# Kernel optimization log

Hardware: AMD Instinct MI355X
Metric: run time of the kernel (lower is better)

## Reference

```python
import jax, jax.numpy as jnp
import numpy as np

B, H, W, C = 4, 256, 256, 256
WS = 8          # window size (both dims)
HEADS = 1
SEQ = WS * WS   # 64 tokens per window
NW = B * (H // WS) * (W // WS)  # 4096 windows
INNER = C * HEADS


def setup_inputs() -> dict:
    key = jax.random.key(0)
    k1, k2, k3, k4 = jax.random.split(key, 4)
    x = jax.random.normal(k1, (B, H, W, C), dtype=jnp.float32)
    attn = jax.random.uniform(k2, (NW, HEADS, SEQ, SEQ), dtype=jnp.float32)
    # to_v: Linear(dim, inner_dim, bias=False); stored as [in, out] for x @ Wv
    Wv = jax.random.normal(k3, (C, INNER), dtype=jnp.float32) * (C ** -0.5)
    # to_out: Linear(inner_dim, dim)
    Wo = jax.random.normal(k4, (INNER, C), dtype=jnp.float32) * (INNER ** -0.5)
    bo = jnp.zeros((C,), dtype=jnp.float32)
    return {"x": x, "attn": attn, "Wv": Wv, "Wo": Wo, "bo": bo}


def reference(x, attn, Wv, Wo, bo):
    b, h, w, c = x.shape
    nh, nw = h // WS, w // WS
    # window partition: b (h b0) (w b1) c -> (b h w) (b0 b1) c
    xw = x.reshape(b, nh, WS, nw, WS, c).transpose(0, 1, 3, 2, 4, 5)
    xw = xw.reshape(b * nh * nw, SEQ, c)
    # value projection, split heads: n s (h d) -> n h s d
    v = (xw @ Wv).reshape(-1, SEQ, HEADS, c).transpose(0, 2, 1, 3)
    # precomputed-attention weighted sum
    out = jnp.einsum('nhij,nhjd->nhid', attn, v)
    # merge heads: n h s d -> n s (h d)
    out = out.transpose(0, 2, 1, 3).reshape(-1, SEQ, HEADS * c)
    out = out @ Wo + bo
    # window un-partition: (b h w) (b0 b1) c -> b (h b0) (w b1) c
    out = out.reshape(b, nh, nw, WS, WS, c).transpose(0, 1, 3, 2, 4, 5)
    return out.reshape(b, h, w, c)
```

## Files before the change

kernel.cpp:

```cpp
#include <hip/hip_runtime.h>
#include <hip/hip_bf16.h>


typedef __bf16 bf16x8 __attribute__((ext_vector_type(8)));
typedef __bf16 bf16x4 __attribute__((ext_vector_type(4)));
typedef float  f32x16 __attribute__((ext_vector_type(16)));
typedef float  f32x4  __attribute__((ext_vector_type(4)));
typedef unsigned int uint;
typedef uint   uint4v __attribute__((ext_vector_type(4)));

#define MFMA32(a, b, c) __builtin_amdgcn_mfma_f32_32x32x16_bf16(a, b, c, 0, 0, 0)

__global__ void wfuse_kernel(const float* __restrict__ Wv,
                             const float* __restrict__ Wo,
                             __bf16* __restrict__ WT) {
  const int n = blockIdx.x;
  const int k = threadIdx.x;
  const float* wvrow = Wv + k * 256;
  float acc = 0.f;
#pragma unroll 4
  for (int j = 0; j < 256; j += 4) {
    f32x4 wv = *(const f32x4*)(wvrow + j);
    acc += wv.x * Wo[(j + 0) * 256 + n];
    acc += wv.y * Wo[(j + 1) * 256 + n];
    acc += wv.z * Wo[(j + 2) * 256 + n];
    acc += wv.w * Wo[(j + 3) * 256 + n];
  }
  WT[n * 256 + k] = (__bf16)acc;
}

static __device__ __forceinline__ uint pkbf(float lo, float hi) {
  return (uint)__builtin_bit_cast(unsigned short, (__bf16)lo) |
         ((uint)__builtin_bit_cast(unsigned short, (__bf16)hi) << 16);
}

static __device__ __forceinline__ void build_bfrags(const f32x16 acc, int lh,
                                                    bf16x8* bf) {
  uint wd0 = pkbf(acc[0],  acc[1]);
  uint wd1 = pkbf(acc[2],  acc[3]);
  uint wd2 = pkbf(acc[4],  acc[5]);
  uint wd3 = pkbf(acc[6],  acc[7]);
  uint wd4 = pkbf(acc[8],  acc[9]);
  uint wd5 = pkbf(acc[10], acc[11]);
  uint wd6 = pkbf(acc[12], acc[13]);
  uint wd7 = pkbf(acc[14], acc[15]);
  {
    uint o0 = (uint)__shfl_xor((int)wd2, 32);
    uint o1 = (uint)__shfl_xor((int)wd3, 32);
    uint o2 = (uint)__shfl_xor((int)wd0, 32);
    uint o3 = (uint)__shfl_xor((int)wd1, 32);
    uint4v uv = { lh ? o0 : wd0, lh ? o1 : wd1,
                  lh ? wd2 : o2, lh ? wd3 : o3 };
    bf[0] = __builtin_bit_cast(bf16x8, uv);
  }
  {
    uint o0 = (uint)__shfl_xor((int)wd6, 32);
    uint o1 = (uint)__shfl_xor((int)wd7, 32);
    uint o2 = (uint)__shfl_xor((int)wd4, 32);
    uint o3 = (uint)__shfl_xor((int)wd5, 32);
    uint4v uv = { lh ? o0 : wd4, lh ? o1 : wd5,
                  lh ? wd6 : o2, lh ? wd7 : o3 };
    bf[1] = __builtin_bit_cast(bf16x8, uv);
  }
}

static __device__ __forceinline__ long wbase(int w) {
  int wi = w & 31;
  int hi = (w >> 5) & 31;
  int b  = w >> 10;
  return (((long)(b * 256 + hi * 8)) * 256 + wi * 8) * 256;
}

static __device__ __forceinline__ void dma16(const float* gp, char* lp) {
  __builtin_amdgcn_global_load_lds(
      (const __attribute__((address_space(1))) uint*)gp,
      (__attribute__((address_space(3))) uint*)lp, 16, 0, 0);
}

static __device__ __forceinline__ bf16x8 ldax_h(const char* xs, int tok, int g) {
  const int sw = tok & 31;
  f32x4 u = *(const f32x4*)(xs + tok * 512 + ((g ^ sw) << 4));
  f32x4 v = *(const f32x4*)(xs + tok * 512 + (((g + 1) ^ sw) << 4));
  bf16x8 r;
  r[0] = (__bf16)u.x; r[1] = (__bf16)u.y; r[2] = (__bf16)u.z; r[3] = (__bf16)u.w;
  r[4] = (__bf16)v.x; r[5] = (__bf16)v.y; r[6] = (__bf16)v.z; r[7] = (__bf16)v.w;
  return r;
}

__global__ __launch_bounds__(512, 2)
void na_msa_kernel(const float* __restrict__ x,
                   const float* __restrict__ attn,
                   const __bf16* __restrict__ WT,
                   const float* __restrict__ bo,
                   float* __restrict__ out) {
  __shared__ char lds[81920];

  const int t    = threadIdx.x;
  const int lane = t & 63;
  const int wvi  = t >> 6;
  const int ln31 = lane & 31;
  const int lh   = lane >> 5;

  const __bf16* wtp = WT + (wvi * 32 + ln31) * 256 + 8 * lh;
  const float bv = bo[wvi * 32 + ln31];

  const int arow0 = t >> 4;
  const int ak0   = (t & 15) * 4;

  const int w0 = blockIdx.x * 8;

#define STAGE_XH(W, HALF, BUFOFF) do {                                     \
    const float* xp_ = x + wbase(W);                                       \
    _Pragma("unroll")                                                      \
    for (int jj = 0; jj < 4; ++jj) {                                       \
      int tp_ = jj * 8 + wvi;                                              \
      int tok_ = tp_ * 2 + (lane >> 5);                                    \
      int perm_ = (lane & 31) ^ (tok_ & 31);                               \
      const float* gp_ = xp_ + (tok_ >> 3) * 65536 + (tok_ & 7) * 256 +    \
                         (HALF) * 128 + perm_ * 4;                         \
      int off_ = __builtin_amdgcn_readfirstlane((BUFOFF) + tp_ * 1024);    \
      dma16(gp_, lds + off_);                                              \
    } } while (0)

#define AWR(BAT, R0, R1) do {                                              \
    *(bf16x4*)((BAT) + arow0 * 128 + ((ak0 * 2) ^ ((arow0 & 7) << 4))) =   \
        bf16x4{ (__bf16)(R0).x, (__bf16)(R0).y, (__bf16)(R0).z, (__bf16)(R0).w }; \
    int row1_ = 32 + arow0;                                                \
    *(bf16x4*)((BAT) + row1_ * 128 + ((ak0 * 2) ^ ((row1_ & 7) << 4))) =   \
        bf16x4{ (__bf16)(R1).x, (__bf16)(R1).y, (__bf16)(R1).z, (__bf16)(R1).w }; \
    } while (0)

  bf16x8 wb[16];
#pragma unroll
  for (int ks = 0; ks < 16; ++ks) wb[ks] = *(const bf16x8*)(wtp + ks * 16);

  {
    const float* ap = attn + (long)w0 * 4096;
    f32x4 a0 = *(const f32x4*)(ap + t * 4);
    f32x4 a1 = *(const f32x4*)(ap + (512 + t) * 4);
    STAGE_XH(w0, 0, 0);
    AWR(lds + 65536, a0, a1);
  }
  asm volatile("s_waitcnt vmcnt(0) lgkmcnt(0)" ::: "memory");
  __builtin_amdgcn_s_barrier();
  __builtin_amdgcn_sched_barrier(0);

#pragma unroll 1
  for (int i = 0; i < 8; ++i) {
    const int w = w0 + i;
    const char* as = lds + 65536 + (i & 1) * 8192;

    f32x4 ra0, ra1;
    if (i < 7) {
      const float* ap = attn + (long)(w + 1) * 4096;
      ra0 = *(const f32x4*)(ap + t * 4);
      ra1 = *(const f32x4*)(ap + (512 + t) * 4);
    }
    STAGE_XH(w, 1, 32768);
    __builtin_amdgcn_sched_barrier(0);

    f32x16 acc0 = {}, acc1 = {};
#pragma unroll
    for (int ks = 0; ks < 8; ++ks) {
      int g = 4 * ks + 2 * lh;
      bf16x8 a0 = ldax_h(lds, ln31, g);
      bf16x8 a1 = ldax_h(lds, 32 + ln31, g);
      acc0 = MFMA32(a0, wb[ks], acc0);
      acc1 = MFMA32(a1, wb[ks], acc1);
    }
    asm volatile("s_waitcnt vmcnt(0) lgkmcnt(0)" ::: "memory");
    __builtin_amdgcn_s_barrier();
    __builtin_amdgcn_sched_barrier(0);

    if (i < 7) STAGE_XH(w + 1, 0, 0);
    __builtin_amdgcn_sched_barrier(0);

#pragma unroll
    for (int ks = 8; ks < 16; ++ks) {
      int g = 4 * (ks - 8) + 2 * lh;
      bf16x8 a0 = ldax_h(lds + 32768, ln31, g);
      bf16x8 a1 = ldax_h(lds + 32768, 32 + ln31, g);
      acc0 = MFMA32(a0, wb[ks], acc0);
      acc1 = MFMA32(a1, wb[ks], acc1);
    }

    bf16x8 bfr[4];
    build_bfrags(acc0, lh, &bfr[0]);
    build_bfrags(acc1, lh, &bfr[2]);

    if (i < 7) {
      AWR(lds + 65536 + ((i + 1) & 1) * 8192, ra0, ra1);
    }

    float* op = out + wbase(w);
    const int ch = wvi * 32 + ln31;

    {
      f32x16 o0 = {};
#pragma unroll
      for (int ks = 0; ks < 4; ++ks) {
        int kk = ks * 16 + 8 * lh;
        int ab0 = ln31 * 128 + ((kk * 2) ^ ((ln31 & 7) << 4));
        bf16x8 a0 = *(const bf16x8*)(as + ab0);
        o0 = MFMA32(a0, bfr[ks], o0);
      }
#pragma unroll
      for (int r = 0; r < 16; ++r) {
        int tok = (r & 3) + 8 * (r >> 2) + 4 * lh;
        op[(tok >> 3) * 65536 + (tok & 7) * 256 + ch] = o0[r] + bv;
      }
    }
    {
      f32x16 o1 = {};
#pragma unroll
      for (int ks = 0; ks < 4; ++ks) {
        int kk = ks * 16 + 8 * lh;
        int ab0 = ln31 * 128 + ((kk * 2) ^ ((ln31 & 7) << 4));
        bf16x8 a1 = *(const bf16x8*)(as + ab0 + 4096);
        o1 = MFMA32(a1, bfr[ks], o1);
      }
#pragma unroll
      for (int r = 0; r < 16; ++r) {
        int tok = 32 + (r & 3) + 8 * (r >> 2) + 4 * lh;
        op[(tok >> 3) * 65536 + (tok & 7) * 256 + ch] = o1[r] + bv;
      }
    }

    asm volatile("s_waitcnt vmcnt(32) lgkmcnt(0)" ::: "memory");
    __builtin_amdgcn_s_barrier();
    __builtin_amdgcn_sched_barrier(0);
  }
#undef STAGE_XH
#undef AWR
}

extern "C" void kernel_launch(void* const* d_in, const int* in_sizes, int n_in,
                              void* d_out, int out_size, void* d_ws, size_t ws_size,
                              hipStream_t stream) {
  const float* x    = (const float*)d_in[0];
  const float* attn = (const float*)d_in[1];
  const float* Wv   = (const float*)d_in[2];
  const float* Wo   = (const float*)d_in[3];
  const float* bo   = (const float*)d_in[4];
  float* out = (float*)d_out;
  __bf16* WT = (__bf16*)d_ws;

  wfuse_kernel<<<256, 256, 0, stream>>>(Wv, Wo, WT);
  na_msa_kernel<<<512, 512, 0, stream>>>(x, attn, WT, bo, out);
}
```

Measured before the change: 151.3 us.

## Triple-buffer x halves and DMA attn into LDS, 16 windows per block

Replaces the register-staged attention load with direct global-to-LDS DMA kept in fp32 and converted to bf16 at read time. The x half-tiles now rotate through three LDS buffers, so the next window's prefetch overlaps more of the current compute, with tuned vmcnt waits. Each block processes 16 windows over half as many blocks, and LDS grows to 128KB. This likely allows only one block per CU, lowering occupancy, and adds fp32-to-bf16 conversion work on the attention operand reads.

```diff
diff --git a/kernel.cpp b/kernel.cpp
--- a/kernel.cpp
+++ b/kernel.cpp
@@ -3,7 +3,6 @@
 
 
 typedef __bf16 bf16x8 __attribute__((ext_vector_type(8)));
-typedef __bf16 bf16x4 __attribute__((ext_vector_type(4)));
 typedef float  f32x16 __attribute__((ext_vector_type(16)));
 typedef float  f32x4  __attribute__((ext_vector_type(4)));
 typedef unsigned int uint;
@@ -32,6 +31,13 @@
 static __device__ __forceinline__ uint pkbf(float lo, float hi) {
   return (uint)__builtin_bit_cast(unsigned short, (__bf16)lo) |
          ((uint)__builtin_bit_cast(unsigned short, (__bf16)hi) << 16);
+}
+
+static __device__ __forceinline__ bf16x8 cvt8(f32x4 u, f32x4 v) {
+  bf16x8 r;
+  r[0] = (__bf16)u.x; r[1] = (__bf16)u.y; r[2] = (__bf16)u.z; r[3] = (__bf16)u.w;
+  r[4] = (__bf16)v.x; r[5] = (__bf16)v.y; r[6] = (__bf16)v.z; r[7] = (__bf16)v.w;
+  return r;
 }
 
 static __device__ __forceinline__ void build_bfrags(const f32x16 acc, int lh,
@@ -81,10 +87,14 @@
   const int sw = tok & 31;
   f32x4 u = *(const f32x4*)(xs + tok * 512 + ((g ^ sw) << 4));
   f32x4 v = *(const f32x4*)(xs + tok * 512 + (((g + 1) ^ sw) << 4));
-  bf16x8 r;
-  r[0] = (__bf16)u.x; r[1] = (__bf16)u.y; r[2] = (__bf16)u.z; r[3] = (__bf16)u.w;
-  r[4] = (__bf16)v.x; r[5] = (__bf16)v.y; r[6] = (__bf16)v.z; r[7] = (__bf16)v.w;
-  return r;
+  return cvt8(u, v);
+}
+
+static __device__ __forceinline__ bf16x8 ldat(const char* as, int row, int g) {
+  const int sw = row & 15;
+  f32x4 u = *(const f32x4*)(as + row * 256 + ((g ^ sw) << 4));
+  f32x4 v = *(const f32x4*)(as + row * 256 + (((g + 1) ^ sw) << 4));
+  return cvt8(u, v);
 }
 
 __global__ __launch_bounds__(512, 2)
@@ -93,7 +103,7 @@
                    const __bf16* __restrict__ WT,
                    const float* __restrict__ bo,
                    float* __restrict__ out) {
-  __shared__ char lds[81920];
+  __shared__ char lds[131072];
 
   const int t    = threadIdx.x;
   const int lane = t & 63;
@@ -104,10 +114,7 @@
   const __bf16* wtp = WT + (wvi * 32 + ln31) * 256 + 8 * lh;
   const float bv = bo[wvi * 32 + ln31];
 
-  const int arow0 = t >> 4;
-  const int ak0   = (t & 15) * 4;
-
-  const int w0 = blockIdx.x * 8;
+  const int w0 = blockIdx.x * 16;
 
 #define STAGE_XH(W, HALF, BUFOFF) do {                                     \
     const float* xp_ = x + wbase(W);                                       \
@@ -122,64 +129,69 @@
       dma16(gp_, lds + off_);                                              \
     } } while (0)
 
-#define AWR(BAT, R0, R1) do {                                              \
-    *(bf16x4*)((BAT) + arow0 * 128 + ((ak0 * 2) ^ ((arow0 & 7) << 4))) =   \
-        bf16x4{ (__bf16)(R0).x, (__bf16)(R0).y, (__bf16)(R0).z, (__bf16)(R0).w }; \
-    int row1_ = 32 + arow0;                                                \
-    *(bf16x4*)((BAT) + row1_ * 128 + ((ak0 * 2) ^ ((row1_ & 7) << 4))) =   \
-        bf16x4{ (__bf16)(R1).x, (__bf16)(R1).y, (__bf16)(R1).z, (__bf16)(R1).w }; \
-    } while (0)
+#define STAGE_AT(W, BUFOFF) do {                                           \
+    const float* ap_ = attn + (long)(W) * 4096;                            \
+    _Pragma("unroll")                                                      \
+    for (int jj = 0; jj < 2; ++jj) {                                       \
+      int j_ = wvi * 2 + jj;                                               \
+      int row_ = j_ * 4 + (lane >> 4);                                     \
+      int g_ = (lane & 15) ^ (row_ & 15);                                  \
+      const float* gp_ = ap_ + row_ * 64 + g_ * 4;                         \
+      int off_ = __builtin_amdgcn_readfirstlane((BUFOFF) + j_ * 1024);     \
+      dma16(gp_, lds + off_);                                              \
+    } } while (0)
 
   bf16x8 wb[16];
 #pragma unroll
   for (int ks = 0; ks < 16; ++ks) wb[ks] = *(const bf16x8*)(wtp + ks * 16);
 
-  {
-    const float* ap = attn + (long)w0 * 4096;
-    f32x4 a0 = *(const f32x4*)(ap + t * 4);
-    f32x4 a1 = *(const f32x4*)(ap + (512 + t) * 4);
-    STAGE_XH(w0, 0, 0);
-    AWR(lds + 65536, a0, a1);
-  }
+  STAGE_XH(w0, 0, 0);
+  STAGE_AT(w0, 98304);
+  STAGE_XH(w0, 1, 32768);
   asm volatile("s_waitcnt vmcnt(0) lgkmcnt(0)" ::: "memory");
   __builtin_amdgcn_s_barrier();
   __builtin_amdgcn_sched_barrier(0);
 
+  int rA = 0, rB = 32768, rC = 65536;
+
 #pragma unroll 1
-  for (int i = 0; i < 8; ++i) {
+  for (int i = 0; i < 16; ++i) {
     const int w = w0 + i;
-    const char* as = lds + 65536 + (i & 1) * 8192;
-
-    f32x4 ra0, ra1;
-    if (i < 7) {
-      const float* ap = attn + (long)(w + 1) * 4096;
-      ra0 = *(const f32x4*)(ap + t * 4);
-      ra1 = *(const f32x4*)(ap + (512 + t) * 4);
-    }
-    STAGE_XH(w, 1, 32768);
+    const char* xsA = lds + rA;
+    const char* xsB = lds + rB;
+    const char* as  = lds + 98304 + (i & 1) * 16384;
+
+    if (i < 15) {
+      STAGE_XH(w + 1, 0, rC);
+      STAGE_AT(w + 1, 98304 + ((i + 1) & 1) * 16384);
+    }
     __builtin_amdgcn_sched_barrier(0);
 
     f32x16 acc0 = {}, acc1 = {};
 #pragma unroll
     for (int ks = 0; ks < 8; ++ks) {
       int g = 4 * ks + 2 * lh;
-      bf16x8 a0 = ldax_h(lds, ln31, g);
-      bf16x8 a1 = ldax_h(lds, 32 + ln31, g);
+      bf16x8 a0 = ldax_h(xsA, ln31, g);
+      bf16x8 a1 = ldax_h(xsA, 32 + ln31, g);
       acc0 = MFMA32(a0, wb[ks], acc0);
       acc1 = MFMA32(a1, wb[ks], acc1);
     }
-    asm volatile("s_waitcnt vmcnt(0) lgkmcnt(0)" ::: "memory");
+    if (i < 15) {
+      asm volatile("s_waitcnt vmcnt(38) lgkmcnt(0)" ::: "memory");
+    } else {
+      asm volatile("s_waitcnt vmcnt(32) lgkmcnt(0)" ::: "memory");
+    }
     __builtin_amdgcn_s_barrier();
     __builtin_amdgcn_sched_barrier(0);
 
-    if (i < 7) STAGE_XH(w + 1, 0, 0);
+    if (i < 15) STAGE_XH(w + 1, 1, rA);
     __builtin_amdgcn_sched_barrier(0);
 
 #pragma unroll
     for (int ks = 8; ks < 16; ++ks) {
       int g = 4 * (ks - 8) + 2 * lh;
-      bf16x8 a0 = ldax_h(lds + 32768, ln31, g);
-      bf16x8 a1 = ldax_h(lds + 32768, 32 + ln31, g);
+      bf16x8 a0 = ldax_h(xsB, ln31, g);
+      bf16x8 a1 = ldax_h(xsB, 32 + ln31, g);
       acc0 = MFMA32(a0, wb[ks], acc0);
       acc1 = MFMA32(a1, wb[ks], acc1);
     }
@@ -188,10 +200,6 @@
     build_bfrags(acc0, lh, &bfr[0]);
     build_bfrags(acc1, lh, &bfr[2]);
 
-    if (i < 7) {
-      AWR(lds + 65536 + ((i + 1) & 1) * 8192, ra0, ra1);
-    }
-
     float* op = out + wbase(w);
     const int ch = wvi * 32 + ln31;
 
@@ -199,10 +207,8 @@
       f32x16 o0 = {};
 #pragma unroll
       for (int ks = 0; ks < 4; ++ks) {
-        int kk = ks * 16 + 8 * lh;
-        int ab0 = ln31 * 128 + ((kk * 2) ^ ((ln31 & 7) << 4));
-        bf16x8 a0 = *(const bf16x8*)(as + ab0);
-        o0 = MFMA32(a0, bfr[ks], o0);
+        int g = 4 * ks + 2 * lh;
+        o0 = MFMA32(ldat(as, ln31, g), bfr[ks], o0);
       }
 #pragma unroll
       for (int r = 0; r < 16; ++r) {
@@ -214,10 +220,8 @@
       f32x16 o1 = {};
 #pragma unroll
       for (int ks = 0; ks < 4; ++ks) {
-        int kk = ks * 16 + 8 * lh;
-        int ab0 = ln31 * 128 + ((kk * 2) ^ ((ln31 & 7) << 4));
-        bf16x8 a1 = *(const bf16x8*)(as + ab0 + 4096);
-        o1 = MFMA32(a1, bfr[ks], o1);
+        int g = 4 * ks + 2 * lh;
+        o1 = MFMA32(ldat(as, 32 + ln31, g), bfr[ks], o1);
       }
 #pragma unroll
       for (int r = 0; r < 16; ++r) {
@@ -226,12 +230,16 @@
       }
     }
 
-    asm volatile("s_waitcnt vmcnt(32) lgkmcnt(0)" ::: "memory");
-    __builtin_amdgcn_s_barrier();
-    __builtin_amdgcn_sched_barrier(0);
+    if (i < 15) {
+      asm volatile("s_waitcnt vmcnt(36) lgkmcnt(0)" ::: "memory");
+      __builtin_amdgcn_s_barrier();
+      __builtin_amdgcn_sched_barrier(0);
+    }
+
+    int tmp = rC; rC = rB; rB = rA; rA = tmp;
   }
 #undef STAGE_XH
-#undef AWR
+#undef STAGE_AT
 }
 
 extern "C" void kernel_launch(void* const* d_in, const int* in_sizes, int n_in,
@@ -246,5 +254,5 @@
   __bf16* WT = (__bf16*)d_ws;
 
   wfuse_kernel<<<256, 256, 0, stream>>>(Wv, Wo, WT);
-  na_msa_kernel<<<512, 512, 0, stream>>>(x, attn, WT, bo, out);
-}
+  na_msa_kernel<<<256, 512, 0, stream>>>(x, attn, WT, bo, out);
+}
```

Result: slower. 157.9 us (+4.4%).
